# Optimization experiments

Measured on AMD Instinct MI355X. Metric: run time of the kernel, lower is better.

The kernel has to match this reference:

```python
import jax, jax.numpy as jnp
import numpy as np

N, T, D, H = 4096, 64, 256, 16


def setup_inputs() -> dict:
    key = jax.random.key(0)
    ks = jax.random.split(key, 6)
    s = 1.0 / np.sqrt(D).astype(np.float32)
    return {
        "x": jax.random.normal(ks[0], (N, T, D), dtype=jnp.float32),
        "pos_emb": jax.random.normal(ks[1], (T, D), dtype=jnp.float32) * s,
        "Wq": jax.random.normal(ks[2], (D, D), dtype=jnp.float32) * s,
        "Wk": jax.random.normal(ks[3], (D, D), dtype=jnp.float32) * s,
        "Wv": jax.random.normal(ks[4], (D, D), dtype=jnp.float32) * s,
        "W_ff": jax.random.normal(ks[5], (D, D), dtype=jnp.float32) * s,
        "b_ff": jnp.zeros((D,), dtype=jnp.float32),
    }


def reference(x, pos_emb, Wq, Wk, Wv, W_ff, b_ff):
    n, t, d = x.shape
    dh = d // H
    # position embedding add (broadcast over nodes)
    h = x + pos_emb[None, :, :]                         # [N,T,D]
    # QKV projections
    q = (h @ Wq).reshape(n, t, H, dh)
    k = (h @ Wk).reshape(n, t, H, dh)
    v = (h @ Wv).reshape(n, t, H, dh)
    # scaled scores; NOTE: original divides by sqrt(num_time_steps), not sqrt(dh)
    scale = jnp.asarray(1.0 / np.sqrt(t), dtype=x.dtype)
    scores = jnp.einsum("nthd,nshd->nhts", q, k) * scale  # [N,H,T,T]
    # causal mask: masked positions get -2^32+1 (as in the TF code)
    causal = jnp.tril(jnp.ones((t, t), dtype=bool))
    neg = jnp.asarray(-(2.0 ** 32) + 1.0, dtype=x.dtype)
    scores = jnp.where(causal[None, None, :, :], scores, neg)
    attn = jax.nn.softmax(scores, axis=-1)
    # attn dropout is identity at inference (tf.layers.dropout training=False)
    out = jnp.einsum("nhts,nshd->nthd", attn, v).reshape(n, t, d)  # merge heads
    # position-wise FFN: kernel-1 conv1d (D->D) + relu, inner residual
    out = jax.nn.relu(out @ W_ff + b_ff) + out
    return out
```

## Files before the change

kernel.cpp:

```cpp
#include <hip/hip_runtime.h>


typedef __attribute__((ext_vector_type(4))) float f32x4;
typedef __attribute__((ext_vector_type(8))) short bf16x8;
typedef __attribute__((ext_vector_type(4))) short bf16x4;

__device__ __forceinline__ short f2bs(float f) {
    union { __bf16 b; short s; } u;
    u.b = (__bf16)f;
    return u.s;
}
__device__ __forceinline__ float b2f(unsigned short s) {
    union { unsigned u; float f; } v; v.u = ((unsigned)s) << 16; return v.f;
}

__global__ void swizzle_w_kernel(const float* __restrict__ Wq,
                                 const float* __restrict__ Wk,
                                 const float* __restrict__ Wv,
                                 const float* __restrict__ Wf,
                                 unsigned short* __restrict__ ws) {
    int tid  = blockIdx.x * 256 + threadIdx.x;
    int mat  = tid >> 13;
    int rem  = tid & 8191;
    int nt   = rem >> 9;
    int ks   = (rem >> 6) & 7;
    int lane = rem & 63;
    const float* W = (mat == 0) ? Wq : (mat == 1) ? Wk : (mat == 2) ? Wv : Wf;
    int n  = nt * 16 + (lane & 15);
    int k0 = ks * 32 + (lane >> 4) * 8;
    bf16x8 o;
#pragma unroll
    for (int j = 0; j < 8; ++j) o[j] = f2bs(W[(k0 + j) * 256 + n]);
    *(bf16x8*)(ws + (size_t)mat * 65536 + (size_t)rem * 8) = o;
}

__global__ __launch_bounds__(512, 4) void fused_node_kernel(
    const float* __restrict__ x, const float* __restrict__ pos,
    const unsigned short* __restrict__ wsw, const float* __restrict__ bff,
    float* __restrict__ out)
{
    __shared__ unsigned short lds_h[64 * 264];

    const int tid  = threadIdx.x;
    const int w    = tid >> 6;
    const int lane = tid & 63;
    const int quad = lane >> 4;
    const int lc   = lane & 15;
    const int node = blockIdx.x;

    {
        const float4* xv = (const float4*)(x + (size_t)node * 16384);
        const float4* pv = (const float4*)pos;
#pragma unroll
        for (int it = 0; it < 8; ++it) {
            int idx = it * 512 + tid;
            float4 a = xv[idx];
            float4 b = pv[idx];
            int row = idx >> 6, c4 = idx & 63;
            ushort4 o;
            o.x = (unsigned short)f2bs(a.x + b.x);
            o.y = (unsigned short)f2bs(a.y + b.y);
            o.z = (unsigned short)f2bs(a.z + b.z);
            o.w = (unsigned short)f2bs(a.w + b.w);
            *(ushort4*)&lds_h[row * 264 + c4 * 4] = o;
        }
    }
    __syncthreads();

    const f32x4 fzero = {0.f, 0.f, 0.f, 0.f};

    const unsigned short* wq_b = wsw;
    const unsigned short* wk_b = wsw + 65536;
    const unsigned short* wv_b = wsw + 131072;
    const unsigned short* wf_b = wsw + 196608;
#define WFRAG(base, mt, ks) (*(const bf16x8*)((base) + (size_t)(((w * 2 + (mt)) * 8 + (ks)) * 64 + lane) * 8))
#define HFRAG(j, ks) (*(const bf16x8*)&lds_h[(16 * (j) + lc) * 264 + (ks) * 32 + quad * 8])

    const float SC = 0.18033688011112042f;

    bf16x4 qf[2][4], kf[2][4], vf[2][4];

#pragma unroll
    for (int h = 0; h < 2; ++h) {
        __builtin_amdgcn_sched_barrier(0);

        f32x4 aq[4], ak[4];
#pragma unroll
        for (int j = 0; j < 4; ++j) { aq[j] = fzero; ak[j] = fzero; }
#pragma unroll
        for (int ks = 0; ks < 8; ++ks) {
            bf16x8 hf[4];
#pragma unroll
            for (int j = 0; j < 4; ++j) hf[j] = HFRAG(j, ks);
            bf16x8 wfq = WFRAG(wq_b, h, ks);
            bf16x8 wfk = WFRAG(wk_b, h, ks);
#pragma unroll
            for (int j = 0; j < 4; ++j) {
                aq[j] = __builtin_amdgcn_mfma_f32_16x16x32_bf16(wfq, hf[j], aq[j], 0, 0, 0);
                ak[j] = __builtin_amdgcn_mfma_f32_16x16x32_bf16(wfk, hf[j], ak[j], 0, 0, 0);
            }
        }
#pragma unroll
        for (int j = 0; j < 4; ++j)
#pragma unroll
            for (int r = 0; r < 4; ++r) {
                qf[h][j][r] = f2bs(aq[j][r]);
                kf[h][j][r] = f2bs(ak[j][r]);
            }

        f32x4 av[4];
#pragma unroll
        for (int i = 0; i < 4; ++i) av[i] = fzero;
#pragma unroll
        for (int ks = 0; ks < 8; ++ks) {
            bf16x8 hf[4];
#pragma unroll
            for (int i = 0; i < 4; ++i) hf[i] = HFRAG(i, ks);
            bf16x8 wfv = WFRAG(wv_b, h, ks);
#pragma unroll
            for (int i = 0; i < 4; ++i)
                av[i] = __builtin_amdgcn_mfma_f32_16x16x32_bf16(hf[i], wfv, av[i], 0, 0, 0);
        }
#pragma unroll
        for (int i = 0; i < 4; ++i)
#pragma unroll
            for (int r = 0; r < 4; ++r) vf[h][i][r] = f2bs(av[i][r]);
    }
    __builtin_amdgcn_sched_barrier(0);

    __syncthreads();

#pragma unroll
    for (int h = 0; h < 2; ++h) {
        __builtin_amdgcn_sched_barrier(0);
#pragma unroll
        for (int i = 0; i < 4; ++i) {
            f32x4 st[4];
#pragma unroll
            for (int js = 0; js <= i; ++js)
                st[js] = __builtin_amdgcn_mfma_f32_16x16x16bf16_1k(kf[h][js], qf[h][i], fzero, 0, 0, 0);
            float sum = 0.f;
#pragma unroll
            for (int js = 0; js <= i; ++js)
#pragma unroll
                for (int r = 0; r < 4; ++r) {
                    float p = __builtin_amdgcn_exp2f(st[js][r] * SC);
                    if (js == i) p = (4 * quad + r <= lc) ? p : 0.0f;
                    st[js][r] = p;
                    sum += p;
                }
            sum += __shfl_xor(sum, 16, 64);
            sum += __shfl_xor(sum, 32, 64);
            float rinv = __builtin_amdgcn_rcpf(sum);

            f32x4 O = fzero;
#pragma unroll
            for (int js = 0; js <= i; ++js) {
                bf16x4 pa;
#pragma unroll
                for (int r = 0; r < 4; ++r) pa[r] = f2bs(st[js][r] * rinv);
                O = __builtin_amdgcn_mfma_f32_16x16x16bf16_1k(pa, vf[h][js], O, 0, 0, 0);
            }
#pragma unroll
            for (int r = 0; r < 4; ++r)
                lds_h[(16 * i + 4 * quad + r) * 264 + w * 32 + h * 16 + lc] =
                    (unsigned short)f2bs(O[r]);
        }
    }

    __syncthreads();

    f32x4 af[4][2];
#pragma unroll
    for (int i = 0; i < 4; ++i)
#pragma unroll
        for (int j = 0; j < 2; ++j) af[i][j] = fzero;
#pragma unroll
    for (int ks = 0; ks < 8; ++ks) {
        bf16x8 hf[4];
#pragma unroll
        for (int i = 0; i < 4; ++i) hf[i] = HFRAG(i, ks);
#pragma unroll
        for (int jn = 0; jn < 2; ++jn) {
            bf16x8 wff = WFRAG(wf_b, jn, ks);
#pragma unroll
            for (int i = 0; i < 4; ++i)
                af[i][jn] = __builtin_amdgcn_mfma_f32_16x16x32_bf16(hf[i], wff, af[i][jn], 0, 0, 0);
        }
    }
    {
        float bias[2];
#pragma unroll
        for (int jn = 0; jn < 2; ++jn) bias[jn] = bff[w * 32 + jn * 16 + lc];
        float* outn = out + (size_t)node * 16384;
#pragma unroll
        for (int i = 0; i < 4; ++i)
#pragma unroll
            for (int jn = 0; jn < 2; ++jn)
#pragma unroll
                for (int r = 0; r < 4; ++r) {
                    int row = i * 16 + quad * 4 + r;
                    int col = w * 32 + jn * 16 + lc;
                    float v = af[i][jn][r] + bias[jn];
                    v = fmaxf(v, 0.0f);
                    v += b2f(lds_h[row * 264 + col]);
                    outn[row * 256 + col] = v;
                }
    }
#undef WFRAG
#undef HFRAG
}

extern "C" void kernel_launch(void* const* d_in, const int* in_sizes, int n_in,
                              void* d_out, int out_size, void* d_ws, size_t ws_size,
                              hipStream_t stream) {
    const float* x   = (const float*)d_in[0];
    const float* pos = (const float*)d_in[1];
    const float* Wq  = (const float*)d_in[2];
    const float* Wk  = (const float*)d_in[3];
    const float* Wv  = (const float*)d_in[4];
    const float* Wf  = (const float*)d_in[5];
    const float* bff = (const float*)d_in[6];
    unsigned short* wsw = (unsigned short*)d_ws;
    float* o = (float*)d_out;

    hipLaunchKernelGGL(swizzle_w_kernel, dim3(128), dim3(256), 0, stream, Wq, Wk, Wv, Wf, wsw);
    hipLaunchKernelGGL(fused_node_kernel, dim3(4096), dim3(512), 0, stream, x, pos, wsw, bff, o);
}
```

Before: 595.1 us.

## Fuse Q/K/V projections per head and use separate LDS buffer for attention output

Computes V alongside Q and K in a single k-loop per head, so each LDS fragment of h is loaded once per head instead of twice. Attention for each head now runs right after its projection, which removes the barrier between the projection and attention phases. Attention output is written to a new second LDS buffer so it no longer overwrites h, at the cost of doubling LDS use per block (about 66KB). That extra LDS may reduce how many blocks fit on a CU.

```diff
diff --git a/kernel.cpp b/kernel.cpp
--- a/kernel.cpp
+++ b/kernel.cpp
@@ -40,6 +40,7 @@
     float* __restrict__ out)
 {
     __shared__ unsigned short lds_h[64 * 264];
+    __shared__ unsigned short lds_o[64 * 264];
 
     const int tid  = threadIdx.x;
     const int w    = tid >> 6;
@@ -75,18 +76,17 @@
     const unsigned short* wf_b = wsw + 196608;
 #define WFRAG(base, mt, ks) (*(const bf16x8*)((base) + (size_t)(((w * 2 + (mt)) * 8 + (ks)) * 64 + lane) * 8))
 #define HFRAG(j, ks) (*(const bf16x8*)&lds_h[(16 * (j) + lc) * 264 + (ks) * 32 + quad * 8])
+#define OFRAG(j, ks) (*(const bf16x8*)&lds_o[(16 * (j) + lc) * 264 + (ks) * 32 + quad * 8])
 
     const float SC = 0.18033688011112042f;
-
-    bf16x4 qf[2][4], kf[2][4], vf[2][4];
 
 #pragma unroll
     for (int h = 0; h < 2; ++h) {
         __builtin_amdgcn_sched_barrier(0);
 
-        f32x4 aq[4], ak[4];
-#pragma unroll
-        for (int j = 0; j < 4; ++j) { aq[j] = fzero; ak[j] = fzero; }
+        f32x4 aq[4], ak[4], av[4];
+#pragma unroll
+        for (int j = 0; j < 4; ++j) { aq[j] = fzero; ak[j] = fzero; av[j] = fzero; }
 #pragma unroll
         for (int ks = 0; ks < 8; ++ks) {
             bf16x8 hf[4];
@@ -94,51 +94,30 @@
             for (int j = 0; j < 4; ++j) hf[j] = HFRAG(j, ks);
             bf16x8 wfq = WFRAG(wq_b, h, ks);
             bf16x8 wfk = WFRAG(wk_b, h, ks);
+            bf16x8 wfv = WFRAG(wv_b, h, ks);
 #pragma unroll
             for (int j = 0; j < 4; ++j) {
                 aq[j] = __builtin_amdgcn_mfma_f32_16x16x32_bf16(wfq, hf[j], aq[j], 0, 0, 0);
                 ak[j] = __builtin_amdgcn_mfma_f32_16x16x32_bf16(wfk, hf[j], ak[j], 0, 0, 0);
+                av[j] = __builtin_amdgcn_mfma_f32_16x16x32_bf16(hf[j], wfv, av[j], 0, 0, 0);
             }
         }
+        bf16x4 qf[4], kf[4], vf[4];
 #pragma unroll
         for (int j = 0; j < 4; ++j)
 #pragma unroll
             for (int r = 0; r < 4; ++r) {
-                qf[h][j][r] = f2bs(aq[j][r]);
-                kf[h][j][r] = f2bs(ak[j][r]);
+                qf[j][r] = f2bs(aq[j][r]);
+                kf[j][r] = f2bs(ak[j][r]);
+                vf[j][r] = f2bs(av[j][r]);
             }
 
-        f32x4 av[4];
-#pragma unroll
-        for (int i = 0; i < 4; ++i) av[i] = fzero;
-#pragma unroll
-        for (int ks = 0; ks < 8; ++ks) {
-            bf16x8 hf[4];
-#pragma unroll
-            for (int i = 0; i < 4; ++i) hf[i] = HFRAG(i, ks);
-            bf16x8 wfv = WFRAG(wv_b, h, ks);
-#pragma unroll
-            for (int i = 0; i < 4; ++i)
-                av[i] = __builtin_amdgcn_mfma_f32_16x16x32_bf16(hf[i], wfv, av[i], 0, 0, 0);
-        }
-#pragma unroll
-        for (int i = 0; i < 4; ++i)
-#pragma unroll
-            for (int r = 0; r < 4; ++r) vf[h][i][r] = f2bs(av[i][r]);
-    }
-    __builtin_amdgcn_sched_barrier(0);
-
-    __syncthreads();
-
-#pragma unroll
-    for (int h = 0; h < 2; ++h) {
-        __builtin_amdgcn_sched_barrier(0);
 #pragma unroll
         for (int i = 0; i < 4; ++i) {
             f32x4 st[4];
 #pragma unroll
             for (int js = 0; js <= i; ++js)
-                st[js] = __builtin_amdgcn_mfma_f32_16x16x16bf16_1k(kf[h][js], qf[h][i], fzero, 0, 0, 0);
+                st[js] = __builtin_amdgcn_mfma_f32_16x16x16bf16_1k(kf[js], qf[i], fzero, 0, 0, 0);
             float sum = 0.f;
 #pragma unroll
             for (int js = 0; js <= i; ++js)
@@ -159,11 +138,11 @@
                 bf16x4 pa;
 #pragma unroll
                 for (int r = 0; r < 4; ++r) pa[r] = f2bs(st[js][r] * rinv);
-                O = __builtin_amdgcn_mfma_f32_16x16x16bf16_1k(pa, vf[h][js], O, 0, 0, 0);
+                O = __builtin_amdgcn_mfma_f32_16x16x16bf16_1k(pa, vf[js], O, 0, 0, 0);
             }
 #pragma unroll
             for (int r = 0; r < 4; ++r)
-                lds_h[(16 * i + 4 * quad + r) * 264 + w * 32 + h * 16 + lc] =
+                lds_o[(16 * i + 4 * quad + r) * 264 + w * 32 + h * 16 + lc] =
                     (unsigned short)f2bs(O[r]);
         }
     }
@@ -179,7 +158,7 @@
     for (int ks = 0; ks < 8; ++ks) {
         bf16x8 hf[4];
 #pragma unroll
-        for (int i = 0; i < 4; ++i) hf[i] = HFRAG(i, ks);
+        for (int i = 0; i < 4; ++i) hf[i] = OFRAG(i, ks);
 #pragma unroll
         for (int jn = 0; jn < 2; ++jn) {
             bf16x8 wff = WFRAG(wf_b, jn, ks);
@@ -203,12 +182,13 @@
                     int col = w * 32 + jn * 16 + lc;
                     float v = af[i][jn][r] + bias[jn];
                     v = fmaxf(v, 0.0f);
-                    v += b2f(lds_h[row * 264 + col]);
+                    v += b2f(lds_o[row * 264 + col]);
                     outn[row * 256 + col] = v;
                 }
     }
 #undef WFRAG
 #undef HFRAG
+#undef OFRAG
 }
 
 extern "C" void kernel_launch(void* const* d_in, const int* in_sizes, int n_in,
```

Result: faster. 541.7 us (-9.0%).
